# Optimization experiments

Hardware: AMD Instinct MI355X
Metric: run time of the kernel (lower is better)

The kernel has to match this reference:

```python
import jax, jax.numpy as jnp
import numpy as np

ROPE_BASE = 10000.0
WINDOW = 256  # sliding_window_size


def _rope_cos_sin(seq_len, dim, dtype):
    inv_freq = 1.0 / (ROPE_BASE ** (jnp.arange(0, dim, 2, dtype=jnp.float32) / dim))
    t = jnp.arange(seq_len, dtype=jnp.float32)
    freqs = jnp.outer(t, inv_freq)                 # [S, D/2]
    emb = jnp.concatenate([freqs, freqs], axis=-1) # [S, D]
    return jnp.cos(emb).astype(dtype), jnp.sin(emb).astype(dtype)


def _rotate_half(x):
    d = x.shape[-1] // 2
    return jnp.concatenate([-x[..., d:], x[..., :d]], axis=-1)


def reference(q, k, v):
    # q, k, v: [B, S, H, D]
    B, S, H, D = q.shape
    cos, sin = _rope_cos_sin(S, D, q.dtype)
    cos = cos[None, :, None, :]  # broadcast over batch & heads
    sin = sin[None, :, None, :]
    q = q * cos + _rotate_half(q) * sin
    k = k * cos + _rotate_half(k) * sin

    scale = D ** -0.5
    scores = jnp.einsum('bqhd,bkhd->bhqk', q, k) * scale  # [B, H, S, S]

    # causal + sliding-window mask: allow i - WINDOW <= j <= i
    i = jnp.arange(S)[:, None]
    j = jnp.arange(S)[None, :]
    allowed = (j <= i) & (j >= i - WINDOW)
    neg = jnp.finfo(scores.dtype).min
    scores = jnp.where(allowed[None, None], scores, neg)

    attn = jax.nn.softmax(scores, axis=-1)
    out = jnp.einsum('bhqk,bkhd->bqhd', attn, v)  # [B, S, H, D]
    return out


def setup_inputs() -> dict:
    key = jax.random.key(0)
    kq, kk, kv = jax.random.split(key, 3)
    shape = (2, 2048, 16, 64)
    return {
        'q': jax.random.normal(kq, shape, dtype=jnp.float32),
        'k': jax.random.normal(kk, shape, dtype=jnp.float32),
        'v': jax.random.normal(kv, shape, dtype=jnp.float32),
    }
```

## Files before the change

kernel.cpp:

```cpp
#include <hip/hip_runtime.h>

typedef __attribute__((ext_vector_type(4))) float  f32x4;
typedef __attribute__((ext_vector_type(8))) short  short8v;
typedef __attribute__((ext_vector_type(4))) short  short4v;

constexpr int S_LEN = 2048;
constexpr int HEADS = 16;
constexpr int DDIM  = 64;
constexpr int ROWSZ = HEADS * DDIM;
constexpr float SCALE = 0.125f;
constexpr float NEGV  = -1e30f;
constexpr float RLN   = 0.2878231366242557f;
constexpr float RSTEP = 0.74989420933246f;
constexpr long  CH_ELEMS = 64 * 64;

__device__ __forceinline__ int swz(int row, int d) { return row * 64 + (d ^ ((row & 7) << 3)); }
__device__ __forceinline__ short f2b(float x) {
    unsigned u = __float_as_uint(x);
    return (short)((u + 0x7FFFu + ((u >> 16) & 1u)) >> 16);
}
template <int V> struct IC { static constexpr int value = V; };

#ifdef __has_builtin
#if __has_builtin(__builtin_amdgcn_global_load_lds)
#define HAS_GLDS 1
#endif
#endif
#ifndef HAS_GLDS
#define HAS_GLDS 0
#endif

#if HAS_GLDS
typedef const __attribute__((address_space(1))) void gas_void;
typedef __attribute__((address_space(3))) void las_void;
__device__ __forceinline__ void g2l16(const short* g, short* l) {
    __builtin_amdgcn_global_load_lds((gas_void*)g, (las_void*)l, 16, 0, 0);
}
#endif

__global__ __launch_bounds__(256) void prep_kernel(const float* __restrict__ K,
                                                   const float* __restrict__ V,
                                                   short* __restrict__ kc,
                                                   short* __restrict__ vt) {
    const int bid = blockIdx.x;
    const int sc = bid & 31, bh = bid >> 5;
    const int b = bh >> 4, h = bh & 15;
    const int s0 = sc * 64;
    const int tid = threadIdx.x;

    const float* Kf = K + ((long)b * S_LEN * HEADS + h) * DDIM;
    short* kout = kc + (long)bid * CH_ELEMS;
    #pragma unroll
    for (int r = 0; r < 2; ++r) {
        const int task = tid + r * 256;
        const int srow = task >> 3, d0 = (task & 7) * 4;
        const int s = s0 + srow;
        const long off = (long)s * ROWSZ + d0;
        float4 lo = *(const float4*)(Kf + off);
        float4 hi = *(const float4*)(Kf + off + 32);
        const float* lp = (const float*)&lo; const float* hp = (const float*)&hi;
        float invf = __expf(-(float)d0 * RLN);
        short4v olo, ohi;
        #pragma unroll
        for (int t = 0; t < 4; ++t) {
            float sn, cs; __sincosf((float)s * invf, &sn, &cs);
            olo[t] = f2b(lp[t] * cs - hp[t] * sn);
            ohi[t] = f2b(hp[t] * cs + lp[t] * sn);
            invf *= RSTEP;
        }
        *(short4v*)(kout + srow * 64 + d0)      = olo;
        *(short4v*)(kout + srow * 64 + d0 + 32) = ohi;
    }

    const float* Vf = V + ((long)b * S_LEN * HEADS + h) * DDIM;
    short* vout = vt + (long)bid * CH_ELEMS;
    const int d = tid & 63, sg = tid >> 6;
    #pragma unroll
    for (int u = 0; u < 2; ++u) {
        const int sb2 = (sg + 4 * u) * 8;
        short8v o;
        #pragma unroll
        for (int t = 0; t < 8; ++t)
            o[t] = f2b(Vf[(long)(s0 + sb2 + t) * ROWSZ + d]);
        *(short8v*)(vout + d * 64 + sb2) = o;
    }
}

__global__ __launch_bounds__(256, 4) void fattn4(const float* __restrict__ Q,
                                                 const short* __restrict__ kc,
                                                 const short* __restrict__ vt,
                                                 float* __restrict__ O) {
    __shared__ __align__(16) short q_s[64 * 64];
    __shared__ __align__(16) short kbuf[2][64 * 64];
    __shared__ __align__(16) short vbuf[2][64 * 64];

    const int tid  = threadIdx.x;
    const int wave = tid >> 6, lane = tid & 63;
    const int col  = lane & 15, grp = lane >> 4;

    const int orig = (blockIdx.x & 7) * 128 + (blockIdx.x >> 3);
    const int qt = orig & 31, bh = orig >> 5;
    const int b = bh >> 4, h = bh & 15;
    const int q0 = qt * 64;
    const long bhoff = ((long)b * S_LEN * HEADS + h) * DDIM;

    const float* Qf = Q + bhoff;
    const short* kcb = kc + (long)bh * 32 * CH_ELEMS;
    const short* vtb = vt + (long)bh * 32 * CH_ELEMS;

    const int lcg = ((lane & 7) ^ (lane >> 3)) * 8;

#if HAS_GLDS
    auto issue_chunk = [&](int c, int cur) {
        const long sidx = (long)qt - 4 + c;
        const short* kslab = kcb + sidx * CH_ELEMS;
        const short* vslab = vtb + sidx * CH_ELEMS;
        #pragma unroll
        for (int r = 0; r < 2; ++r) {
            const int row = wave * 8 + r * 32 + (lane >> 3);
            g2l16(kslab + row * 64 + lcg, &kbuf[cur][wave * 512 + r * 2048]);
            g2l16(vslab + row * 64 + lcg, &vbuf[cur][wave * 512 + r * 2048]);
        }
    };
#endif

    const int c0 = (q0 >= 256) ? 0 : ((256 - q0) >> 6);
#if HAS_GLDS
    issue_chunk(c0, 0);
#endif
    #pragma unroll
    for (int r = 0; r < 2; ++r) {
        const int task = tid + r * 256;
        const int row = task >> 3, d0 = (task & 7) * 4;
        const int s = q0 + row;
        const long off = (long)s * ROWSZ + d0;
        float4 lo = *(const float4*)(Qf + off);
        float4 hi = *(const float4*)(Qf + off + 32);
        const float* lp = (const float*)&lo; const float* hp = (const float*)&hi;
        float invf = __expf(-(float)d0 * RLN);
        short4v olo, ohi;
        #pragma unroll
        for (int t = 0; t < 4; ++t) {
            float sn, cs; __sincosf((float)s * invf, &sn, &cs);
            olo[t] = f2b(lp[t] * cs - hp[t] * sn);
            ohi[t] = f2b(hp[t] * cs + lp[t] * sn);
            invf *= RSTEP;
        }
        *(short4v*)&q_s[swz(row, d0)]      = olo;
        *(short4v*)&q_s[swz(row, d0 + 32)] = ohi;
    }
    __syncthreads();

    const short8v qa0 = *(const short8v*)&q_s[swz(wave * 16 + col, grp * 8)];
    const short8v qa1 = *(const short8v*)&q_s[swz(wave * 16 + col, 32 + grp * 8)];
    short* pslice = &q_s[wave * 1024];
    const int qw0 = q0 + wave * 16;

    f32x4 acc[4]; f32x4 lacc = {0.f, 0.f, 0.f, 0.f};
    #pragma unroll
    for (int dt = 0; dt < 4; ++dt) acc[dt] = f32x4{0.f, 0.f, 0.f, 0.f};
    short8v ones;
    #pragma unroll
    for (int t = 0; t < 8; ++t) ones[t] = (short)0x3F80;

    auto body = [&](int cur, int kc0, auto mtag) {
        constexpr int MODE = decltype(mtag)::value;
        const short* kd = kbuf[cur]; const short* vd = vbuf[cur];
        f32x4 sv[4];
        __builtin_amdgcn_s_setprio(1);
        #pragma unroll
        for (int jt = 0; jt < 4; ++jt) {
            short8v b0 = *(const short8v*)&kd[swz(jt * 16 + col, grp * 8)];
            short8v b1 = *(const short8v*)&kd[swz(jt * 16 + col, 32 + grp * 8)];
            f32x4 z = {0.f, 0.f, 0.f, 0.f};
            z      = __builtin_amdgcn_mfma_f32_16x16x32_bf16(qa0, b0, z, 0, 0, 0);
            sv[jt] = __builtin_amdgcn_mfma_f32_16x16x32_bf16(qa1, b1, z, 0, 0, 0);
        }
        __builtin_amdgcn_s_setprio(0);
        #pragma unroll
        for (int jt = 0; jt < 4; ++jt) {
            const int j = kc0 + jt * 16 + col;
            #pragma unroll
            for (int r = 0; r < 4; ++r) {
                float s = sv[jt][r] * SCALE;
                if constexpr (MODE == 1) { if (j + 256 < qw0 + grp * 4 + r) s = NEGV; }
                if constexpr (MODE == 2) { if (j > qw0 + grp * 4 + r) s = NEGV; }
                pslice[swz(grp * 4 + r, jt * 16 + col)] = f2b(__expf(s));
            }
        }
        short8v pa0 = *(const short8v*)&pslice[swz(col, grp * 8)];
        short8v pa1 = *(const short8v*)&pslice[swz(col, 32 + grp * 8)];
        __builtin_amdgcn_s_setprio(1);
        {
            f32x4 z = lacc;
            z    = __builtin_amdgcn_mfma_f32_16x16x32_bf16(pa0, ones, z, 0, 0, 0);
            lacc = __builtin_amdgcn_mfma_f32_16x16x32_bf16(pa1, ones, z, 0, 0, 0);
        }
        #pragma unroll
        for (int dt = 0; dt < 4; ++dt) {
            short8v v0 = *(const short8v*)&vd[swz(dt * 16 + col, grp * 8)];
            short8v v1 = *(const short8v*)&vd[swz(dt * 16 + col, 32 + grp * 8)];
            f32x4 z = acc[dt];
            z       = __builtin_amdgcn_mfma_f32_16x16x32_bf16(pa0, v0, z, 0, 0, 0);
            acc[dt] = __builtin_amdgcn_mfma_f32_16x16x32_bf16(pa1, v1, z, 0, 0, 0);
        }
        __builtin_amdgcn_s_setprio(0);
    };

#if HAS_GLDS
    int cur = 0;
    for (int c = c0; c < 5; ++c) {
        const int kc0 = q0 - 256 + c * 64;
        __syncthreads();
        if (c < 4) issue_chunk(c + 1, cur ^ 1);
        if (c == 0)      body(cur, kc0, IC<1>{});
        else if (c == 4) body(cur, kc0, IC<2>{});
        else             body(cur, kc0, IC<0>{});
        cur ^= 1;
    }
#else
    for (int c = c0; c < 5; ++c) {
        const int kc0 = q0 - 256 + c * 64;
        const long sidx = (long)qt - 4 + c;
        const short* kslab = kcb + sidx * CH_ELEMS;
        const short* vslab = vtb + sidx * CH_ELEMS;
        __syncthreads();
        #pragma unroll
        for (int r = 0; r < 2; ++r) {
            const int p = r * 2048 + tid * 8;
            const int row = p >> 6;
            const int cg = ((tid & 7) ^ (row & 7)) * 8;
            *(short8v*)&kbuf[0][p] = *(const short8v*)(kslab + row * 64 + cg);
            *(short8v*)&vbuf[0][p] = *(const short8v*)(vslab + row * 64 + cg);
        }
        __syncthreads();
        if (c == 0)      body(0, kc0, IC<1>{});
        else if (c == 4) body(0, kc0, IC<2>{});
        else             body(0, kc0, IC<0>{});
    }
#endif

    float* Ob = O + bhoff;
    #pragma unroll
    for (int r = 0; r < 4; ++r) {
        const float inv = 1.0f / lacc[r];
        const int i = qw0 + grp * 4 + r;
        #pragma unroll
        for (int dt = 0; dt < 4; ++dt)
            Ob[(long)i * ROWSZ + dt * 16 + col] = acc[dt][r] * inv;
    }
}

extern "C" void kernel_launch(void* const* d_in, const int* in_sizes, int n_in,
                              void* d_out, int out_size, void* d_ws, size_t ws_size,
                              hipStream_t stream) {
    const float* q = (const float*)d_in[0];
    const float* k = (const float*)d_in[1];
    const float* v = (const float*)d_in[2];
    float* o = (float*)d_out;
    short* kc = (short*)d_ws;
    short* vt = kc + (long)32 * 32 * CH_ELEMS;
    prep_kernel<<<dim3(1024), dim3(256), 0, stream>>>(k, v, kc, vt);
    fattn4<<<dim3(1024), dim3(256), 0, stream>>>(q, kc, vt, o);
}
```

Measured before the change: 107.7 us.

## Move Q RoPE and bf16 conversion into prep kernel, load Q fragments directly

Q's RoPE rotation and bf16 conversion move into the prep kernel, which already computes sin/cos for K at the same positions, so the sincos values are shared. The attention kernel then loads its Q MFMA fragments straight from a precomputed bf16 slab in global memory. This removes the shared-memory Q staging and its barrier. The P scratch tile gets a different swizzle to cut LDS bank conflicts, and the per-chunk barrier moves to the end of the loop. The cost is an extra write and read of a bf16 Q buffer in the workspace.

```diff
diff --git a/kernel.cpp b/kernel.cpp
--- a/kernel.cpp
+++ b/kernel.cpp
@@ -13,8 +13,12 @@
 constexpr float RLN   = 0.2878231366242557f;
 constexpr float RSTEP = 0.74989420933246f;
 constexpr long  CH_ELEMS = 64 * 64;
+constexpr long  NSLAB = 32 * 32;
 
 __device__ __forceinline__ int swz(int row, int d) { return row * 64 + (d ^ ((row & 7) << 3)); }
+__device__ __forceinline__ int pswz(int row, int d) {
+    return row * 64 + (d ^ ((((row & 7) ^ ((row >> 3) << 1)) & 7) << 3));
+}
 __device__ __forceinline__ short f2b(float x) {
     unsigned u = __float_as_uint(x);
     return (short)((u + 0x7FFFu + ((u >> 16) & 1u)) >> 16);
@@ -40,39 +44,61 @@
 
 __global__ __launch_bounds__(256) void prep_kernel(const float* __restrict__ K,
                                                    const float* __restrict__ V,
+                                                   const float* __restrict__ Q,
                                                    short* __restrict__ kc,
-                                                   short* __restrict__ vt) {
+                                                   short* __restrict__ vt,
+                                                   short* __restrict__ qs) {
     const int bid = blockIdx.x;
     const int sc = bid & 31, bh = bid >> 5;
     const int b = bh >> 4, h = bh & 15;
     const int s0 = sc * 64;
     const int tid = threadIdx.x;
-
-    const float* Kf = K + ((long)b * S_LEN * HEADS + h) * DDIM;
+    const long base = ((long)b * S_LEN * HEADS + h) * DDIM;
+
+    const float* Kf = K + base;
+    const float* Qf = Q + base;
     short* kout = kc + (long)bid * CH_ELEMS;
+    short* qout = qs + (long)bid * CH_ELEMS;
+
     #pragma unroll
     for (int r = 0; r < 2; ++r) {
         const int task = tid + r * 256;
         const int srow = task >> 3, d0 = (task & 7) * 4;
         const int s = s0 + srow;
         const long off = (long)s * ROWSZ + d0;
-        float4 lo = *(const float4*)(Kf + off);
-        float4 hi = *(const float4*)(Kf + off + 32);
-        const float* lp = (const float*)&lo; const float* hp = (const float*)&hi;
+        float sn[4], cs[4];
         float invf = __expf(-(float)d0 * RLN);
-        short4v olo, ohi;
-        #pragma unroll
-        for (int t = 0; t < 4; ++t) {
-            float sn, cs; __sincosf((float)s * invf, &sn, &cs);
-            olo[t] = f2b(lp[t] * cs - hp[t] * sn);
-            ohi[t] = f2b(hp[t] * cs + lp[t] * sn);
-            invf *= RSTEP;
-        }
-        *(short4v*)(kout + srow * 64 + d0)      = olo;
-        *(short4v*)(kout + srow * 64 + d0 + 32) = ohi;
-    }
-
-    const float* Vf = V + ((long)b * S_LEN * HEADS + h) * DDIM;
+        #pragma unroll
+        for (int t = 0; t < 4; ++t) { __sincosf((float)s * invf, &sn[t], &cs[t]); invf *= RSTEP; }
+        {
+            float4 lo = *(const float4*)(Kf + off);
+            float4 hi = *(const float4*)(Kf + off + 32);
+            const float* lp = (const float*)&lo; const float* hp = (const float*)&hi;
+            short4v olo, ohi;
+            #pragma unroll
+            for (int t = 0; t < 4; ++t) {
+                olo[t] = f2b(lp[t] * cs[t] - hp[t] * sn[t]);
+                ohi[t] = f2b(hp[t] * cs[t] + lp[t] * sn[t]);
+            }
+            *(short4v*)(kout + srow * 64 + d0)      = olo;
+            *(short4v*)(kout + srow * 64 + d0 + 32) = ohi;
+        }
+        {
+            float4 lo = *(const float4*)(Qf + off);
+            float4 hi = *(const float4*)(Qf + off + 32);
+            const float* lp = (const float*)&lo; const float* hp = (const float*)&hi;
+            short4v olo, ohi;
+            #pragma unroll
+            for (int t = 0; t < 4; ++t) {
+                olo[t] = f2b(lp[t] * cs[t] - hp[t] * sn[t]);
+                ohi[t] = f2b(hp[t] * cs[t] + lp[t] * sn[t]);
+            }
+            *(short4v*)(qout + srow * 64 + d0)      = olo;
+            *(short4v*)(qout + srow * 64 + d0 + 32) = ohi;
+        }
+    }
+
+    const float* Vf = V + base;
     short* vout = vt + (long)bid * CH_ELEMS;
     const int d = tid & 63, sg = tid >> 6;
     #pragma unroll
@@ -86,11 +112,11 @@
     }
 }
 
-__global__ __launch_bounds__(256, 4) void fattn4(const float* __restrict__ Q,
+__global__ __launch_bounds__(256, 4) void fattn6(const short* __restrict__ qs,
                                                  const short* __restrict__ kc,
                                                  const short* __restrict__ vt,
                                                  float* __restrict__ O) {
-    __shared__ __align__(16) short q_s[64 * 64];
+    __shared__ __align__(16) short p_s[4 * 1024];
     __shared__ __align__(16) short kbuf[2][64 * 64];
     __shared__ __align__(16) short vbuf[2][64 * 64];
 
@@ -104,9 +130,9 @@
     const int q0 = qt * 64;
     const long bhoff = ((long)b * S_LEN * HEADS + h) * DDIM;
 
-    const float* Qf = Q + bhoff;
     const short* kcb = kc + (long)bh * 32 * CH_ELEMS;
     const short* vtb = vt + (long)bh * 32 * CH_ELEMS;
+    const short* qslab = qs + ((long)bh * 32 + qt) * CH_ELEMS;
 
     const int lcg = ((lane & 7) ^ (lane >> 3)) * 8;
 
@@ -128,32 +154,10 @@
 #if HAS_GLDS
     issue_chunk(c0, 0);
 #endif
-    #pragma unroll
-    for (int r = 0; r < 2; ++r) {
-        const int task = tid + r * 256;
-        const int row = task >> 3, d0 = (task & 7) * 4;
-        const int s = q0 + row;
-        const long off = (long)s * ROWSZ + d0;
-        float4 lo = *(const float4*)(Qf + off);
-        float4 hi = *(const float4*)(Qf + off + 32);
-        const float* lp = (const float*)&lo; const float* hp = (const float*)&hi;
-        float invf = __expf(-(float)d0 * RLN);
-        short4v olo, ohi;
-        #pragma unroll
-        for (int t = 0; t < 4; ++t) {
-            float sn, cs; __sincosf((float)s * invf, &sn, &cs);
-            olo[t] = f2b(lp[t] * cs - hp[t] * sn);
-            ohi[t] = f2b(hp[t] * cs + lp[t] * sn);
-            invf *= RSTEP;
-        }
-        *(short4v*)&q_s[swz(row, d0)]      = olo;
-        *(short4v*)&q_s[swz(row, d0 + 32)] = ohi;
-    }
-    __syncthreads();
-
-    const short8v qa0 = *(const short8v*)&q_s[swz(wave * 16 + col, grp * 8)];
-    const short8v qa1 = *(const short8v*)&q_s[swz(wave * 16 + col, 32 + grp * 8)];
-    short* pslice = &q_s[wave * 1024];
+    const short8v qa0 = *(const short8v*)(qslab + (wave * 16 + col) * 64 + grp * 8);
+    const short8v qa1 = *(const short8v*)(qslab + (wave * 16 + col) * 64 + 32 + grp * 8);
+
+    short* pslice = &p_s[wave * 1024];
     const int qw0 = q0 + wave * 16;
 
     f32x4 acc[4]; f32x4 lacc = {0.f, 0.f, 0.f, 0.f};
@@ -185,11 +189,11 @@
                 float s = sv[jt][r] * SCALE;
                 if constexpr (MODE == 1) { if (j + 256 < qw0 + grp * 4 + r) s = NEGV; }
                 if constexpr (MODE == 2) { if (j > qw0 + grp * 4 + r) s = NEGV; }
-                pslice[swz(grp * 4 + r, jt * 16 + col)] = f2b(__expf(s));
+                pslice[pswz(grp * 4 + r, jt * 16 + col)] = f2b(__expf(s));
             }
         }
-        short8v pa0 = *(const short8v*)&pslice[swz(col, grp * 8)];
-        short8v pa1 = *(const short8v*)&pslice[swz(col, 32 + grp * 8)];
+        short8v pa0 = *(const short8v*)&pslice[pswz(col, grp * 8)];
+        short8v pa1 = *(const short8v*)&pslice[pswz(col, 32 + grp * 8)];
         __builtin_amdgcn_s_setprio(1);
         {
             f32x4 z = lacc;
@@ -208,15 +212,16 @@
     };
 
 #if HAS_GLDS
+    __syncthreads();
     int cur = 0;
     for (int c = c0; c < 5; ++c) {
         const int kc0 = q0 - 256 + c * 64;
-        __syncthreads();
         if (c < 4) issue_chunk(c + 1, cur ^ 1);
         if (c == 0)      body(cur, kc0, IC<1>{});
         else if (c == 4) body(cur, kc0, IC<2>{});
         else             body(cur, kc0, IC<0>{});
         cur ^= 1;
+        __syncthreads();
     }
 #else
     for (int c = c0; c < 5; ++c) {
@@ -259,7 +264,8 @@
     const float* v = (const float*)d_in[2];
     float* o = (float*)d_out;
     short* kc = (short*)d_ws;
-    short* vt = kc + (long)32 * 32 * CH_ELEMS;
-    prep_kernel<<<dim3(1024), dim3(256), 0, stream>>>(k, v, kc, vt);
-    fattn4<<<dim3(1024), dim3(256), 0, stream>>>(q, kc, vt, o);
-}
+    short* vt = kc + NSLAB * CH_ELEMS;
+    short* qs = vt + NSLAB * CH_ELEMS;
+    prep_kernel<<<dim3(1024), dim3(256), 0, stream>>>(k, v, q, kc, vt, qs);
+    fattn6<<<dim3(1024), dim3(256), 0, stream>>>(qs, kc, vt, o);
+}
```

Result: slower. 113.3 us (+5.2%).

## Compute transposed scores to keep P in registers and drop LDS round-trip

Applied to the files above, without the earlier changes.

Swaps the MFMA operand order so the score tile comes out transposed, letting each lane pack its exp'd probabilities straight into the B operand of the PV MFMA instead of writing P to shared memory and reading it back. The row-sum is now kept as a per-lane scalar reduced with shuffles at the end, replacing the extra MFMA against a ones vector. V fragments are gathered as two short4 loads to match the new layout. The barrier moves to the end of each loop iteration, and the output store is staged through LDS so each lane writes float4 vectors. Risks include extra LDS loads for V and a possible hazard from the moved barrier relative to issue_chunk.

```diff
diff --git a/kernel.cpp b/kernel.cpp
--- a/kernel.cpp
+++ b/kernel.cpp
@@ -13,6 +13,7 @@
 constexpr float RLN   = 0.2878231366242557f;
 constexpr float RSTEP = 0.74989420933246f;
 constexpr long  CH_ELEMS = 64 * 64;
+constexpr long  NSLAB = 32 * 32;
 
 __device__ __forceinline__ int swz(int row, int d) { return row * 64 + (d ^ ((row & 7) << 3)); }
 __device__ __forceinline__ short f2b(float x) {
@@ -86,7 +87,7 @@
     }
 }
 
-__global__ __launch_bounds__(256, 4) void fattn4(const float* __restrict__ Q,
+__global__ __launch_bounds__(256, 4) void fattn7(const float* __restrict__ Q,
                                                  const short* __restrict__ kc,
                                                  const short* __restrict__ vt,
                                                  float* __restrict__ O) {
@@ -153,15 +154,26 @@
 
     const short8v qa0 = *(const short8v*)&q_s[swz(wave * 16 + col, grp * 8)];
     const short8v qa1 = *(const short8v*)&q_s[swz(wave * 16 + col, 32 + grp * 8)];
-    short* pslice = &q_s[wave * 1024];
     const int qw0 = q0 + wave * 16;
-
-    f32x4 acc[4]; f32x4 lacc = {0.f, 0.f, 0.f, 0.f};
+    const int i_mine = qw0 + col;
+
+    f32x4 acc[4];
     #pragma unroll
     for (int dt = 0; dt < 4; ++dt) acc[dt] = f32x4{0.f, 0.f, 0.f, 0.f};
-    short8v ones;
-    #pragma unroll
-    for (int t = 0; t < 8; ++t) ones[t] = (short)0x3F80;
+    float psum = 0.f;
+
+    auto vfrag = [&](const short* vd, int dt, int jtA) -> short8v {
+        const int d = dt * 16 + col;
+        const int sub = (grp & 1) * 4;
+        const int gA = ((jtA * 2 + (grp >> 1)) ^ (d & 7)) << 3;
+        const int gB = (((jtA + 1) * 2 + (grp >> 1)) ^ (d & 7)) << 3;
+        short4v a = *(const short4v*)&vd[d * 64 + gA + sub];
+        short4v bb = *(const short4v*)&vd[d * 64 + gB + sub];
+        short8v r;
+        r[0] = a[0]; r[1] = a[1]; r[2] = a[2]; r[3] = a[3];
+        r[4] = bb[0]; r[5] = bb[1]; r[6] = bb[2]; r[7] = bb[3];
+        return r;
+    };
 
     auto body = [&](int cur, int kc0, auto mtag) {
         constexpr int MODE = decltype(mtag)::value;
@@ -170,39 +182,36 @@
         __builtin_amdgcn_s_setprio(1);
         #pragma unroll
         for (int jt = 0; jt < 4; ++jt) {
-            short8v b0 = *(const short8v*)&kd[swz(jt * 16 + col, grp * 8)];
-            short8v b1 = *(const short8v*)&kd[swz(jt * 16 + col, 32 + grp * 8)];
+            short8v kb0 = *(const short8v*)&kd[swz(jt * 16 + col, grp * 8)];
+            short8v kb1 = *(const short8v*)&kd[swz(jt * 16 + col, 32 + grp * 8)];
             f32x4 z = {0.f, 0.f, 0.f, 0.f};
-            z      = __builtin_amdgcn_mfma_f32_16x16x32_bf16(qa0, b0, z, 0, 0, 0);
-            sv[jt] = __builtin_amdgcn_mfma_f32_16x16x32_bf16(qa1, b1, z, 0, 0, 0);
+            z      = __builtin_amdgcn_mfma_f32_16x16x32_bf16(kb0, qa0, z, 0, 0, 0);
+            sv[jt] = __builtin_amdgcn_mfma_f32_16x16x32_bf16(kb1, qa1, z, 0, 0, 0);
         }
         __builtin_amdgcn_s_setprio(0);
+        short8v pb01, pb23;
         #pragma unroll
         for (int jt = 0; jt < 4; ++jt) {
-            const int j = kc0 + jt * 16 + col;
             #pragma unroll
             for (int r = 0; r < 4; ++r) {
+                const int j = kc0 + jt * 16 + grp * 4 + r;
                 float s = sv[jt][r] * SCALE;
-                if constexpr (MODE == 1) { if (j + 256 < qw0 + grp * 4 + r) s = NEGV; }
-                if constexpr (MODE == 2) { if (j > qw0 + grp * 4 + r) s = NEGV; }
-                pslice[swz(grp * 4 + r, jt * 16 + col)] = f2b(__expf(s));
+                if constexpr (MODE == 1) { if (j + 256 < i_mine) s = NEGV; }
+                if constexpr (MODE == 2) { if (j > i_mine) s = NEGV; }
+                const float p = __expf(s);
+                psum += p;
+                const short pb = f2b(p);
+                if (jt == 0) pb01[r] = pb;
+                else if (jt == 1) pb01[4 + r] = pb;
+                else if (jt == 2) pb23[r] = pb;
+                else pb23[4 + r] = pb;
             }
         }
-        short8v pa0 = *(const short8v*)&pslice[swz(col, grp * 8)];
-        short8v pa1 = *(const short8v*)&pslice[swz(col, 32 + grp * 8)];
         __builtin_amdgcn_s_setprio(1);
-        {
-            f32x4 z = lacc;
-            z    = __builtin_amdgcn_mfma_f32_16x16x32_bf16(pa0, ones, z, 0, 0, 0);
-            lacc = __builtin_amdgcn_mfma_f32_16x16x32_bf16(pa1, ones, z, 0, 0, 0);
-        }
         #pragma unroll
         for (int dt = 0; dt < 4; ++dt) {
-            short8v v0 = *(const short8v*)&vd[swz(dt * 16 + col, grp * 8)];
-            short8v v1 = *(const short8v*)&vd[swz(dt * 16 + col, 32 + grp * 8)];
-            f32x4 z = acc[dt];
-            z       = __builtin_amdgcn_mfma_f32_16x16x32_bf16(pa0, v0, z, 0, 0, 0);
-            acc[dt] = __builtin_amdgcn_mfma_f32_16x16x32_bf16(pa1, v1, z, 0, 0, 0);
+            acc[dt] = __builtin_amdgcn_mfma_f32_16x16x32_bf16(vfrag(vd, dt, 0), pb01, acc[dt], 0, 0, 0);
+            acc[dt] = __builtin_amdgcn_mfma_f32_16x16x32_bf16(vfrag(vd, dt, 2), pb23, acc[dt], 0, 0, 0);
         }
         __builtin_amdgcn_s_setprio(0);
     };
@@ -211,12 +220,12 @@
     int cur = 0;
     for (int c = c0; c < 5; ++c) {
         const int kc0 = q0 - 256 + c * 64;
-        __syncthreads();
         if (c < 4) issue_chunk(c + 1, cur ^ 1);
         if (c == 0)      body(cur, kc0, IC<1>{});
         else if (c == 4) body(cur, kc0, IC<2>{});
         else             body(cur, kc0, IC<0>{});
         cur ^= 1;
+        __syncthreads();
     }
 #else
     for (int c = c0; c < 5; ++c) {
@@ -240,14 +249,23 @@
     }
 #endif
 
-    float* Ob = O + bhoff;
-    #pragma unroll
-    for (int r = 0; r < 4; ++r) {
-        const float inv = 1.0f / lacc[r];
-        const int i = qw0 + grp * 4 + r;
-        #pragma unroll
-        for (int dt = 0; dt < 4; ++dt)
-            Ob[(long)i * ROWSZ + dt * 16 + col] = acc[dt][r] * inv;
+    {
+        float l = psum;
+        l += __shfl_xor(l, 16, 64);
+        l += __shfl_xor(l, 32, 64);
+        const float inv = 1.0f / l;
+
+        float* tb = reinterpret_cast<float*>(q_s) + wave * 320;
+        float* Ob = O + bhoff;
+        const int ri = lane >> 2, rc = (lane & 3) * 4;
+        #pragma unroll
+        for (int dt = 0; dt < 4; ++dt) {
+            #pragma unroll
+            for (int r = 0; r < 4; ++r)
+                tb[col * 20 + grp * 4 + r] = acc[dt][r] * inv;
+            f32x4 o = *(const f32x4*)&tb[ri * 20 + rc];
+            *(f32x4*)&Ob[(long)(qw0 + ri) * ROWSZ + dt * 16 + rc] = o;
+        }
     }
 }
 
@@ -259,7 +277,7 @@
     const float* v = (const float*)d_in[2];
     float* o = (float*)d_out;
     short* kc = (short*)d_ws;
-    short* vt = kc + (long)32 * 32 * CH_ELEMS;
+    short* vt = kc + NSLAB * CH_ELEMS;
     prep_kernel<<<dim3(1024), dim3(256), 0, stream>>>(k, v, kc, vt);
-    fattn4<<<dim3(1024), dim3(256), 0, stream>>>(q, kc, vt, o);
-}
+    fattn7<<<dim3(1024), dim3(256), 0, stream>>>(q, kc, vt, o);
+}
```

Measured after the change: 108.1 us. No clear change (+0.4%).
